# Optimization experiments

Hardware: AMD Instinct MI355X
Metric: run time of the kernel (lower is better)

## Reference

```python
import jax, jax.numpy as jnp
import numpy as np

N0, N1, NB = 247808, 22528, 2048
E0, E1 = 225280, 20480
C = 256
EW = 600000

def setup_inputs() -> dict:
    key = jax.random.key(0)
    ks = jax.random.split(key, 16)
    s = 1.0 / np.sqrt(C)
    return {
        "x": jax.random.normal(ks[0], (N0, C), dtype=jnp.float32),
        "src0": jax.random.randint(ks[1], (E0,), 0, N0),
        "dst0": jax.random.randint(ks[2], (E0,), 0, N1),
        "eid0": jax.random.randint(ks[3], (E0,), 0, EW),
        "src1": jax.random.randint(ks[4], (E1,), 0, N1),
        "dst1": jax.random.randint(ks[5], (E1,), 0, NB),
        "eid1": jax.random.randint(ks[6], (E1,), 0, EW),
        "edge_weight": jax.random.uniform(ks[7], (EW,), dtype=jnp.float32),
        "W_rel0": jax.random.uniform(ks[8], (C, C), jnp.float32, -s, s),
        "b0": jax.random.uniform(ks[9], (C,), jnp.float32, -s, s),
        "W_root0": jax.random.uniform(ks[10], (C, C), jnp.float32, -s, s),
        "W_rel1": jax.random.uniform(ks[11], (C, C), jnp.float32, -s, s),
        "b1": jax.random.uniform(ks[12], (C,), jnp.float32, -s, s),
        "W_root1": jax.random.uniform(ks[13], (C, C), jnp.float32, -s, s),
    }

def graph_conv(x, src, dst, ew, n_dst, W_rel, b, W_root):
    # PyG GraphConv, aggr='mean', bipartite: out_i = W_rel * mean_j(e_ji * x_j) + W_root * x_i + b
    msg = ew[:, None] * x[src]                                   # [E, C]
    agg = jax.ops.segment_sum(msg, dst, num_segments=n_dst)      # [n_dst, C]
    cnt = jax.ops.segment_sum(jnp.ones_like(ew), dst, num_segments=n_dst)
    mean = agg / jnp.maximum(cnt, 1.0)[:, None]
    return mean @ W_rel + b + x[:n_dst] @ W_root

def reference(x, src0, dst0, eid0, src1, dst1, eid1, edge_weight,
              W_rel0, b0, W_root0, W_rel1, b1, W_root1):
    h = graph_conv(x, src0, dst0, edge_weight[eid0], N1, W_rel0, b0, W_root0)
    h = jax.nn.relu(h)  # dropout is identity in eval mode
    h = graph_conv(h, src1, dst1, edge_weight[eid1], NB, W_rel1, b1, W_root1)
    return h, jax.nn.log_softmax(h, axis=1)
```

## Files before the change

kernel.cpp:

```cpp
#include <hip/hip_runtime.h>
#include <cstdint>
#include <cmath>

#define N0c 247808
#define N1c 22528
#define NBc 2048
#define E0c 225280
#define E1c 20480
#define Cc  256
#define NDST (N1c + NBc)
#define ETOT (E0c + E1c)

typedef __attribute__((ext_vector_type(8))) short short8;
typedef __attribute__((ext_vector_type(4))) float floatx4;

__device__ inline unsigned short f2bf(float f) {
    union { float f; unsigned u; } cv; cv.f = f;
    unsigned u = cv.u;
    u += 0x7fffu + ((u >> 16) & 1u);
    return (unsigned short)(u >> 16);
}

__global__ void count_both(const int* __restrict__ dst0, const int* __restrict__ dst1,
                           int* __restrict__ cnt) {
    int e = blockIdx.x * blockDim.x + threadIdx.x;
    if (e < E0c) atomicAdd(&cnt[dst0[e]], 1);
    else if (e < ETOT) atomicAdd(&cnt[N1c + dst1[e - E0c]], 1);
}

__global__ __launch_bounds__(256) void scan_part(const int* __restrict__ in,
                                                 int* __restrict__ out,
                                                 int* __restrict__ partials) {
    __shared__ int wsum[4];
    int t = threadIdx.x, lane = t & 63, w = t >> 6;
    int base = blockIdx.x * 1024 + t * 4;
    int4 v = *(const int4*)(in + base);
    int s = v.x + v.y + v.z + v.w;
    int incl = s;
#pragma unroll
    for (int o = 1; o < 64; o <<= 1) {
        int u = __shfl_up(incl, o);
        if (lane >= o) incl += u;
    }
    if (lane == 63) wsum[w] = incl;
    __syncthreads();
    int woff = 0;
    for (int j = 0; j < w; j++) woff += wsum[j];
    int excl = woff + incl - s;
    int4 o4;
    o4.x = excl; excl += v.x;
    o4.y = excl; excl += v.y;
    o4.z = excl; excl += v.z;
    o4.w = excl; excl += v.w;
    *(int4*)(out + base) = o4;
    if (t == 255) partials[blockIdx.x] = woff + incl;
}

__global__ void scan_partials(int* __restrict__ partials, int* __restrict__ total, int np) {
    int t = threadIdx.x;
    int v = (t < np) ? partials[t] : 0;
    int incl = v;
#pragma unroll
    for (int o = 1; o < 64; o <<= 1) {
        int u = __shfl_up(incl, o);
        if (t >= o) incl += u;
    }
    if (t < np) partials[t] = incl - v;
    if (t == 63) total[0] = incl;
}

__global__ __launch_bounds__(256) void scan_add(int* __restrict__ off, int* __restrict__ cur,
                                                const int* __restrict__ partials) {
    int t = threadIdx.x;
    int base = blockIdx.x * 1024 + t * 4;
    int p = partials[blockIdx.x];
    int4 v = *(const int4*)(off + base);
    v.x += p; v.y += p; v.z += p; v.w += p;
    *(int4*)(off + base) = v;
    *(int4*)(cur + base) = v;
}

__global__ void fill_both(const int* __restrict__ src0, const int* __restrict__ dst0,
                          const int* __restrict__ eid0,
                          const int* __restrict__ src1, const int* __restrict__ dst1,
                          const int* __restrict__ eid1,
                          const float* __restrict__ ew,
                          int* __restrict__ cur, int* __restrict__ srcs,
                          float* __restrict__ wsr) {
    int e = blockIdx.x * blockDim.x + threadIdx.x;
    if (e < E0c) {
        int p = atomicAdd(&cur[dst0[e]], 1);
        srcs[p] = src0[e];
        wsr[p] = ew[eid0[e]];
    } else if (e < ETOT) {
        int i = e - E0c;
        int p = atomicAdd(&cur[N1c + dst1[i]], 1);
        srcs[p] = src1[i];
        wsr[p] = ew[eid1[i]];
    }
}

__global__ void pack_W(const float* __restrict__ Wrel0, const float* __restrict__ Wroot0,
                       const float* __restrict__ Wrel1, const float* __restrict__ Wroot1,
                       short* __restrict__ Wp0, short* __restrict__ Wp1) {
    int gid = blockIdx.x * blockDim.x + threadIdx.x;
    int lane = gid & 63;
    int kt = (gid >> 6) & 15;
    int nt = (gid >> 10) & 15;
    int layer = gid >> 14;
    const float* Wrel  = layer ? Wrel1  : Wrel0;
    const float* Wroot = layer ? Wroot1 : Wroot0;
    short* Wp = layer ? Wp1 : Wp0;
    int nn = nt * 16 + (lane & 15);
    int kb = kt * 32 + (lane >> 4) * 8;
    unsigned short frag[8];
#pragma unroll
    for (int j = 0; j < 8; j++) {
        int k = kb + j;
        float f = (k < 256) ? Wrel[k * 256 + nn] : Wroot[(k - 256) * 256 + nn];
        frag[j] = f2bf(f);
    }
    short8 v;
#pragma unroll
    for (int j = 0; j < 8; j++) v[j] = (short)frag[j];
    *(short8*)(Wp + (((size_t)nt * 16 + kt) * 64 + lane) * 8) = v;
}

__global__ __launch_bounds__(256) void convert_root(const float* __restrict__ x,
                                                    short* __restrict__ A0) {
    int gid = blockIdx.x * blockDim.x + threadIdx.x;
    int row = gid >> 6, lane = gid & 63;
    float4 v = *(const float4*)(x + (size_t)row * Cc + lane * 4);
    ushort4 o;
    o.x = f2bf(v.x); o.y = f2bf(v.y); o.z = f2bf(v.z); o.w = f2bf(v.w);
    *(ushort4*)(A0 + (size_t)row * 512 + 256 + lane * 4) = o;
}

__global__ __launch_bounds__(256) void gather_mean_bf16(const float* __restrict__ feat,
                                                        const int* __restrict__ off,
                                                        const int* __restrict__ srcs,
                                                        const float* __restrict__ wsr,
                                                        short* __restrict__ outA,
                                                        int baseRow, int nrows) {
    int wid  = (blockIdx.x * blockDim.x + threadIdx.x) >> 6;
    int lane = threadIdx.x & 63;
    if (wid >= nrows) return;
    int crow = baseRow + wid;
    int s = off[crow], e = off[crow + 1];
    float4 acc = make_float4(0.f, 0.f, 0.f, 0.f);
    int i = s;
    for (; i + 1 < e; i += 2) {
        int   s0 = srcs[i], s1 = srcs[i + 1];
        float w0 = wsr[i],  w1 = wsr[i + 1];
        float4 v0 = ((const float4*)(feat + (size_t)s0 * Cc))[lane];
        float4 v1 = ((const float4*)(feat + (size_t)s1 * Cc))[lane];
        acc.x += w0 * v0.x + w1 * v1.x;
        acc.y += w0 * v0.y + w1 * v1.y;
        acc.z += w0 * v0.z + w1 * v1.z;
        acc.w += w0 * v0.w + w1 * v1.w;
    }
    if (i < e) {
        int sid = srcs[i];
        float w = wsr[i];
        float4 v = ((const float4*)(feat + (size_t)sid * Cc))[lane];
        acc.x += w * v.x; acc.y += w * v.y; acc.z += w * v.z; acc.w += w * v.w;
    }
    float inv = 1.0f / fmaxf((float)(e - s), 1.0f);
    ushort4 o;
    o.x = f2bf(acc.x * inv); o.y = f2bf(acc.y * inv);
    o.z = f2bf(acc.z * inv); o.w = f2bf(acc.w * inv);
    *(ushort4*)(outA + (size_t)wid * 512 + lane * 4) = o;
}

template <bool RELU, bool EXTRA>
__global__ __launch_bounds__(256) void gemm_mfma(const short* __restrict__ A,
                                                 const short* __restrict__ Wp,
                                                 const float* __restrict__ bias,
                                                 float* __restrict__ out,
                                                 short* __restrict__ extra) {
    __shared__ short As[32 * 520];
    int t = threadIdx.x;
    int base = blockIdx.x * 32;
#pragma unroll
    for (int it = 0; it < 8; it++) {
        int idx = it * 256 + t;
        int row = idx >> 6, c = idx & 63;
        short8 v = *(const short8*)(A + (size_t)(base + row) * 512 + c * 8);
        *(short8*)(&As[row * 520 + c * 8]) = v;
    }
    __syncthreads();

    int lane = t & 63, w = t >> 6;
    int l15 = lane & 15, lq = lane >> 4;
    floatx4 acc[2][4];
#pragma unroll
    for (int rt = 0; rt < 2; rt++)
#pragma unroll
        for (int ct = 0; ct < 4; ct++) acc[rt][ct] = (floatx4){0.f, 0.f, 0.f, 0.f};

    for (int kt = 0; kt < 16; kt++) {
        short8 a0 = *(const short8*)(&As[l15 * 520 + kt * 32 + lq * 8]);
        short8 a1 = *(const short8*)(&As[(16 + l15) * 520 + kt * 32 + lq * 8]);
#pragma unroll
        for (int ct = 0; ct < 4; ct++) {
            int nt = w * 4 + ct;
            short8 b = *(const short8*)(Wp + (((size_t)nt * 16 + kt) * 64 + lane) * 8);
            acc[0][ct] = __builtin_amdgcn_mfma_f32_16x16x32_bf16(a0, b, acc[0][ct], 0, 0, 0);
            acc[1][ct] = __builtin_amdgcn_mfma_f32_16x16x32_bf16(a1, b, acc[1][ct], 0, 0, 0);
        }
    }

#pragma unroll
    for (int rt = 0; rt < 2; rt++)
#pragma unroll
        for (int ct = 0; ct < 4; ct++) {
            int col = (w * 4 + ct) * 16 + l15;
            float bv = bias[col];
#pragma unroll
            for (int r = 0; r < 4; r++) {
                int row = base + rt * 16 + lq * 4 + r;
                float val = acc[rt][ct][r] + bv;
                if (RELU) val = fmaxf(val, 0.f);
                out[(size_t)row * Cc + col] = val;
                if (EXTRA) {
                    if (row < NBc) extra[(size_t)row * 512 + 256 + col] = (short)f2bf(val);
                }
            }
        }
}

__global__ void log_softmax_k(const float* __restrict__ in, float* __restrict__ out) {
    int gid  = blockIdx.x * blockDim.x + threadIdx.x;
    int row  = gid >> 6;
    int lane = threadIdx.x & 63;
    float4 v = ((const float4*)(in + (size_t)row * Cc))[lane];
    float m = fmaxf(fmaxf(v.x, v.y), fmaxf(v.z, v.w));
#pragma unroll
    for (int o = 32; o; o >>= 1) m = fmaxf(m, __shfl_xor(m, o));
    float s = expf(v.x - m) + expf(v.y - m) + expf(v.z - m) + expf(v.w - m);
#pragma unroll
    for (int o = 32; o; o >>= 1) s += __shfl_xor(s, o);
    float lse = m + logf(s);
    float4 o4;
    o4.x = v.x - lse; o4.y = v.y - lse; o4.z = v.z - lse; o4.w = v.w - lse;
    ((float4*)(out + (size_t)row * Cc))[lane] = o4;
}

extern "C" void kernel_launch(void* const* d_in, const int* in_sizes, int n_in,
                              void* d_out, int out_size, void* d_ws, size_t ws_size,
                              hipStream_t stream) {
    const float* x     = (const float*)d_in[0];
    const int*   src0  = (const int*)d_in[1];
    const int*   dst0  = (const int*)d_in[2];
    const int*   eid0  = (const int*)d_in[3];
    const int*   src1  = (const int*)d_in[4];
    const int*   dst1  = (const int*)d_in[5];
    const int*   eid1  = (const int*)d_in[6];
    const float* ew    = (const float*)d_in[7];
    const float* Wrel0 = (const float*)d_in[8];
    const float* b0    = (const float*)d_in[9];
    const float* Wroot0= (const float*)d_in[10];
    const float* Wrel1 = (const float*)d_in[11];
    const float* b1    = (const float*)d_in[12];
    const float* Wroot1= (const float*)d_in[13];

    char* wsb = (char*)d_ws;
    size_t o = 0;
    auto alloc = [&](size_t bytes) { void* p = wsb + o; o += (bytes + 15) & ~(size_t)15; return p; };
    int*   off   = (int*)  alloc((NDST + 1) * 4);
    int*   cnt   = (int*)  alloc(NDST * 4);
    int*   srcs  = (int*)  alloc(ETOT * 4);
    float* wsr   = (float*)alloc(ETOT * 4);
    int*   parts = (int*)  alloc(64 * 4);
    short* Wp0   = (short*)alloc(16 * 16 * 64 * 8 * 2);
    short* Wp1   = (short*)alloc(16 * 16 * 64 * 8 * 2);
    short* A0    = (short*)alloc((size_t)N1c * 512 * 2);
    short* A1    = (short*)alloc((size_t)NBc * 512 * 2);
    float* h     = (float*)alloc((size_t)N1c * Cc * 4);

    hipMemsetAsync(cnt, 0, NDST * sizeof(int), stream);
    count_both<<<ETOT / 256, 256, 0, stream>>>(dst0, dst1, cnt);
    scan_part<<<NDST / 1024, 256, 0, stream>>>(cnt, off, parts);
    scan_partials<<<1, 64, 0, stream>>>(parts, off + NDST, NDST / 1024);
    scan_add<<<NDST / 1024, 256, 0, stream>>>(off, cnt, parts);
    fill_both<<<ETOT / 256, 256, 0, stream>>>(src0, dst0, eid0, src1, dst1, eid1,
                                              ew, cnt, srcs, wsr);

    pack_W<<<32768 / 256, 256, 0, stream>>>(Wrel0, Wroot0, Wrel1, Wroot1, Wp0, Wp1);
    convert_root<<<(N1c * 64) / 256, 256, 0, stream>>>(x, A0);

    gather_mean_bf16<<<(N1c * 64) / 256, 256, 0, stream>>>(x, off, srcs, wsr, A0, 0, N1c);
    gemm_mfma<true, true><<<N1c / 32, 256, 0, stream>>>(A0, Wp0, b0, h, A1);

    gather_mean_bf16<<<(NBc * 64) / 256, 256, 0, stream>>>(h, off, srcs, wsr, A1, N1c, NBc);
    float* out2 = (float*)d_out;
    gemm_mfma<false, false><<<NBc / 32, 256, 0, stream>>>(A1, Wp1, b1, out2, nullptr);

    log_softmax_k<<<(NBc * 64) / 256, 256, 0, stream>>>(out2, out2 + (size_t)NBc * Cc);
}
```

Measured before the change: 445.3 us.

## Fuse prep kernels, scan partials, root conversion and log-softmax to cut launches

Merges the edge-count and weight-packing kernels into one launch. The partial-sum scan moves into scan_add, the root-feature bf16 conversion moves into the first gather, and log_softmax is folded into the final GEMM epilogue through shared memory. The gather loop is also unrolled to four edges per iteration. The aim is to remove several small kernel launches and one extra pass over the output; the cost is a little redundant scan work per block and an extra barrier in the GEMM.

After: 442.5 us. Within noise of the previous version (-0.6%).

```diff
diff --git a/kernel.cpp b/kernel.cpp
--- a/kernel.cpp
+++ b/kernel.cpp
@@ -21,11 +21,36 @@
     return (unsigned short)(u >> 16);
 }
 
-__global__ void count_both(const int* __restrict__ dst0, const int* __restrict__ dst1,
-                           int* __restrict__ cnt) {
-    int e = blockIdx.x * blockDim.x + threadIdx.x;
-    if (e < E0c) atomicAdd(&cnt[dst0[e]], 1);
-    else if (e < ETOT) atomicAdd(&cnt[N1c + dst1[e - E0c]], 1);
+__global__ __launch_bounds__(256) void prep_kernel(
+    const int* __restrict__ dst0, const int* __restrict__ dst1, int* __restrict__ cnt,
+    const float* __restrict__ Wrel0, const float* __restrict__ Wroot0,
+    const float* __restrict__ Wrel1, const float* __restrict__ Wroot1,
+    short* __restrict__ Wp0, short* __restrict__ Wp1) {
+    int b = blockIdx.x;
+    if (b < ETOT / 256) {
+        int e = b * 256 + threadIdx.x;
+        if (e < E0c) atomicAdd(&cnt[dst0[e]], 1);
+        else         atomicAdd(&cnt[N1c + dst1[e - E0c]], 1);
+    } else {
+        int gid = (b - ETOT / 256) * 256 + threadIdx.x;
+        int lane = gid & 63;
+        int kt = (gid >> 6) & 15;
+        int nt = (gid >> 10) & 15;
+        int layer = gid >> 14;
+        const float* Wrel  = layer ? Wrel1  : Wrel0;
+        const float* Wroot = layer ? Wroot1 : Wroot0;
+        short* Wp = layer ? Wp1 : Wp0;
+        int nn = nt * 16 + (lane & 15);
+        int kb = kt * 32 + (lane >> 4) * 8;
+        short8 v;
+#pragma unroll
+        for (int j = 0; j < 8; j++) {
+            int k = kb + j;
+            float f = (k < 256) ? Wrel[k * 256 + nn] : Wroot[(k - 256) * 256 + nn];
+            v[j] = (short)f2bf(f);
+        }
+        *(short8*)(Wp + (((size_t)nt * 16 + kt) * 64 + lane) * 8) = v;
+    }
 }
 
 __global__ __launch_bounds__(256) void scan_part(const int* __restrict__ in,
@@ -56,24 +81,24 @@
     if (t == 255) partials[blockIdx.x] = woff + incl;
 }
 
-__global__ void scan_partials(int* __restrict__ partials, int* __restrict__ total, int np) {
-    int t = threadIdx.x;
-    int v = (t < np) ? partials[t] : 0;
-    int incl = v;
-#pragma unroll
-    for (int o = 1; o < 64; o <<= 1) {
-        int u = __shfl_up(incl, o);
-        if (t >= o) incl += u;
-    }
-    if (t < np) partials[t] = incl - v;
-    if (t == 63) total[0] = incl;
-}
-
 __global__ __launch_bounds__(256) void scan_add(int* __restrict__ off, int* __restrict__ cur,
                                                 const int* __restrict__ partials) {
+    __shared__ int pfx_s;
     int t = threadIdx.x;
+    if (t < 32) {
+        int v = (t < NDST / 1024) ? partials[t] : 0;
+        int incl = v;
+#pragma unroll
+        for (int o = 1; o < 32; o <<= 1) {
+            int u = __shfl_up(incl, o);
+            if (t >= o) incl += u;
+        }
+        if (t == (int)blockIdx.x) pfx_s = incl - v;
+        if (blockIdx.x == 0 && t == NDST / 1024 - 1) off[NDST] = incl;
+    }
+    __syncthreads();
+    int p = pfx_s;
     int base = blockIdx.x * 1024 + t * 4;
-    int p = partials[blockIdx.x];
     int4 v = *(const int4*)(off + base);
     v.x += p; v.y += p; v.z += p; v.w += p;
     *(int4*)(off + base) = v;
@@ -100,42 +125,7 @@
     }
 }
 
-__global__ void pack_W(const float* __restrict__ Wrel0, const float* __restrict__ Wroot0,
-                       const float* __restrict__ Wrel1, const float* __restrict__ Wroot1,
-                       short* __restrict__ Wp0, short* __restrict__ Wp1) {
-    int gid = blockIdx.x * blockDim.x + threadIdx.x;
-    int lane = gid & 63;
-    int kt = (gid >> 6) & 15;
-    int nt = (gid >> 10) & 15;
-    int layer = gid >> 14;
-    const float* Wrel  = layer ? Wrel1  : Wrel0;
-    const float* Wroot = layer ? Wroot1 : Wroot0;
-    short* Wp = layer ? Wp1 : Wp0;
-    int nn = nt * 16 + (lane & 15);
-    int kb = kt * 32 + (lane >> 4) * 8;
-    unsigned short frag[8];
-#pragma unroll
-    for (int j = 0; j < 8; j++) {
-        int k = kb + j;
-        float f = (k < 256) ? Wrel[k * 256 + nn] : Wroot[(k - 256) * 256 + nn];
-        frag[j] = f2bf(f);
-    }
-    short8 v;
-#pragma unroll
-    for (int j = 0; j < 8; j++) v[j] = (short)frag[j];
-    *(short8*)(Wp + (((size_t)nt * 16 + kt) * 64 + lane) * 8) = v;
-}
-
-__global__ __launch_bounds__(256) void convert_root(const float* __restrict__ x,
-                                                    short* __restrict__ A0) {
-    int gid = blockIdx.x * blockDim.x + threadIdx.x;
-    int row = gid >> 6, lane = gid & 63;
-    float4 v = *(const float4*)(x + (size_t)row * Cc + lane * 4);
-    ushort4 o;
-    o.x = f2bf(v.x); o.y = f2bf(v.y); o.z = f2bf(v.z); o.w = f2bf(v.w);
-    *(ushort4*)(A0 + (size_t)row * 512 + 256 + lane * 4) = o;
-}
-
+template <bool ROOT>
 __global__ __launch_bounds__(256) void gather_mean_bf16(const float* __restrict__ feat,
                                                         const int* __restrict__ off,
                                                         const int* __restrict__ srcs,
@@ -149,17 +139,19 @@
     int s = off[crow], e = off[crow + 1];
     float4 acc = make_float4(0.f, 0.f, 0.f, 0.f);
     int i = s;
-    for (; i + 1 < e; i += 2) {
-        int   s0 = srcs[i], s1 = srcs[i + 1];
-        float w0 = wsr[i],  w1 = wsr[i + 1];
+    for (; i + 3 < e; i += 4) {
+        int   s0 = srcs[i],     s1 = srcs[i + 1], s2 = srcs[i + 2], s3 = srcs[i + 3];
+        float w0 = wsr[i],      w1 = wsr[i + 1],  w2 = wsr[i + 2],  w3 = wsr[i + 3];
         float4 v0 = ((const float4*)(feat + (size_t)s0 * Cc))[lane];
         float4 v1 = ((const float4*)(feat + (size_t)s1 * Cc))[lane];
-        acc.x += w0 * v0.x + w1 * v1.x;
-        acc.y += w0 * v0.y + w1 * v1.y;
-        acc.z += w0 * v0.z + w1 * v1.z;
-        acc.w += w0 * v0.w + w1 * v1.w;
-    }
-    if (i < e) {
+        float4 v2 = ((const float4*)(feat + (size_t)s2 * Cc))[lane];
+        float4 v3 = ((const float4*)(feat + (size_t)s3 * Cc))[lane];
+        acc.x += w0 * v0.x + w1 * v1.x + w2 * v2.x + w3 * v3.x;
+        acc.y += w0 * v0.y + w1 * v1.y + w2 * v2.y + w3 * v3.y;
+        acc.z += w0 * v0.z + w1 * v1.z + w2 * v2.z + w3 * v3.z;
+        acc.w += w0 * v0.w + w1 * v1.w + w2 * v2.w + w3 * v3.w;
+    }
+    for (; i < e; i++) {
         int sid = srcs[i];
         float w = wsr[i];
         float4 v = ((const float4*)(feat + (size_t)sid * Cc))[lane];
@@ -170,14 +162,21 @@
     o.x = f2bf(acc.x * inv); o.y = f2bf(acc.y * inv);
     o.z = f2bf(acc.z * inv); o.w = f2bf(acc.w * inv);
     *(ushort4*)(outA + (size_t)wid * 512 + lane * 4) = o;
-}
-
-template <bool RELU, bool EXTRA>
+    if (ROOT) {
+        float4 r = ((const float4*)(feat + (size_t)crow * Cc))[lane];
+        ushort4 ro;
+        ro.x = f2bf(r.x); ro.y = f2bf(r.y); ro.z = f2bf(r.z); ro.w = f2bf(r.w);
+        *(ushort4*)(outA + (size_t)wid * 512 + 256 + lane * 4) = ro;
+    }
+}
+
+template <bool RELU, bool EXTRA, bool SMAX>
 __global__ __launch_bounds__(256) void gemm_mfma(const short* __restrict__ A,
                                                  const short* __restrict__ Wp,
                                                  const float* __restrict__ bias,
                                                  float* __restrict__ out,
-                                                 short* __restrict__ extra) {
+                                                 short* __restrict__ extra,
+                                                 float* __restrict__ out1) {
     __shared__ short As[32 * 520];
     int t = threadIdx.x;
     int base = blockIdx.x * 32;
@@ -210,6 +209,9 @@
         }
     }
 
+    float* Ls = (float*)As;
+    if (SMAX) __syncthreads();
+
 #pragma unroll
     for (int rt = 0; rt < 2; rt++)
 #pragma unroll
@@ -218,32 +220,35 @@
             float bv = bias[col];
 #pragma unroll
             for (int r = 0; r < 4; r++) {
-                int row = base + rt * 16 + lq * 4 + r;
+                int rl = rt * 16 + lq * 4 + r;
+                int row = base + rl;
                 float val = acc[rt][ct][r] + bv;
                 if (RELU) val = fmaxf(val, 0.f);
                 out[(size_t)row * Cc + col] = val;
                 if (EXTRA) {
                     if (row < NBc) extra[(size_t)row * 512 + 256 + col] = (short)f2bf(val);
                 }
+                if (SMAX) Ls[rl * 260 + col] = val;
             }
         }
-}
-
-__global__ void log_softmax_k(const float* __restrict__ in, float* __restrict__ out) {
-    int gid  = blockIdx.x * blockDim.x + threadIdx.x;
-    int row  = gid >> 6;
-    int lane = threadIdx.x & 63;
-    float4 v = ((const float4*)(in + (size_t)row * Cc))[lane];
-    float m = fmaxf(fmaxf(v.x, v.y), fmaxf(v.z, v.w));
-#pragma unroll
-    for (int o = 32; o; o >>= 1) m = fmaxf(m, __shfl_xor(m, o));
-    float s = expf(v.x - m) + expf(v.y - m) + expf(v.z - m) + expf(v.w - m);
-#pragma unroll
-    for (int o = 32; o; o >>= 1) s += __shfl_xor(s, o);
-    float lse = m + logf(s);
-    float4 o4;
-    o4.x = v.x - lse; o4.y = v.y - lse; o4.z = v.z - lse; o4.w = v.w - lse;
-    ((float4*)(out + (size_t)row * Cc))[lane] = o4;
+
+    if (SMAX) {
+        __syncthreads();
+        for (int rr = 0; rr < 8; rr++) {
+            int rl = w * 8 + rr;
+            float4 v = *(const float4*)(Ls + rl * 260 + lane * 4);
+            float m = fmaxf(fmaxf(v.x, v.y), fmaxf(v.z, v.w));
+#pragma unroll
+            for (int o = 32; o; o >>= 1) m = fmaxf(m, __shfl_xor(m, o));
+            float s = expf(v.x - m) + expf(v.y - m) + expf(v.z - m) + expf(v.w - m);
+#pragma unroll
+            for (int o = 32; o; o >>= 1) s += __shfl_xor(s, o);
+            float lse = m + logf(s);
+            float4 o4;
+            o4.x = v.x - lse; o4.y = v.y - lse; o4.z = v.z - lse; o4.w = v.w - lse;
+            *(float4*)(out1 + (size_t)(base + rl) * Cc + lane * 4) = o4;
+        }
+    }
 }
 
 extern "C" void kernel_launch(void* const* d_in, const int* in_sizes, int n_in,
@@ -279,22 +284,18 @@
     float* h     = (float*)alloc((size_t)N1c * Cc * 4);
 
     hipMemsetAsync(cnt, 0, NDST * sizeof(int), stream);
-    count_both<<<ETOT / 256, 256, 0, stream>>>(dst0, dst1, cnt);
+    prep_kernel<<<ETOT / 256 + 128, 256, 0, stream>>>(dst0, dst1, cnt,
+                                                      Wrel0, Wroot0, Wrel1, Wroot1, Wp0, Wp1);
     scan_part<<<NDST / 1024, 256, 0, stream>>>(cnt, off, parts);
-    scan_partials<<<1, 64, 0, stream>>>(parts, off + NDST, NDST / 1024);
     scan_add<<<NDST / 1024, 256, 0, stream>>>(off, cnt, parts);
     fill_both<<<ETOT / 256, 256, 0, stream>>>(src0, dst0, eid0, src1, dst1, eid1,
                                               ew, cnt, srcs, wsr);
 
-    pack_W<<<32768 / 256, 256, 0, stream>>>(Wrel0, Wroot0, Wrel1, Wroot1, Wp0, Wp1);
-    convert_root<<<(N1c * 64) / 256, 256, 0, stream>>>(x, A0);
-
-    gather_mean_bf16<<<(N1c * 64) / 256, 256, 0, stream>>>(x, off, srcs, wsr, A0, 0, N1c);
-    gemm_mfma<true, true><<<N1c / 32, 256, 0, stream>>>(A0, Wp0, b0, h, A1);
-
-    gather_mean_bf16<<<(NBc * 64) / 256, 256, 0, stream>>>(h, off, srcs, wsr, A1, N1c, NBc);
+    gather_mean_bf16<true><<<(N1c * 64) / 256, 256, 0, stream>>>(x, off, srcs, wsr, A0, 0, N1c);
+    gemm_mfma<true, true, false><<<N1c / 32, 256, 0, stream>>>(A0, Wp0, b0, h, A1, nullptr);
+
+    gather_mean_bf16<false><<<(NBc * 64) / 256, 256, 0, stream>>>(h, off, srcs, wsr, A1, N1c, NBc);
     float* out2 = (float*)d_out;
-    gemm_mfma<false, false><<<NBc / 32, 256, 0, stream>>>(A1, Wp1, b1, out2, nullptr);
-
-    log_softmax_k<<<(NBc * 64) / 256, 256, 0, stream>>>(out2, out2 + (size_t)NBc * Cc);
-}
+    gemm_mfma<false, false, true><<<NBc / 32, 256, 0, stream>>>(A1, Wp1, b1, out2, nullptr,
+                                                                out2 + (size_t)NBc * Cc);
+}
```
